# Kernel tuning notes

Hardware: AMD Instinct MI355X
Metric: run time of the kernel (lower is better)

Reference implementation:

```python
import jax, jax.numpy as jnp
import numpy as np

NUM_HEADS = 4


def setup_inputs() -> dict:
    key = jax.random.key(0)
    ks = jax.random.split(key, 5)
    B, C, L = 8, 128, 2048
    x = jax.random.normal(ks[0], (B, C, L), dtype=jnp.float32)
    # Conv1d(C, 3C, 1) == per-position linear; weight [3C, C], bias [3C]
    w_qkv = jax.random.normal(ks[1], (3 * C, C), dtype=jnp.float32) * (1.0 / np.sqrt(C))
    b_qkv = jax.random.normal(ks[2], (3 * C,), dtype=jnp.float32) * 0.01
    w_proj = jax.random.normal(ks[3], (C, C), dtype=jnp.float32) * (1.0 / np.sqrt(C))
    b_proj = jax.random.normal(ks[4], (C,), dtype=jnp.float32) * 0.01
    return {"x": x, "w_qkv": w_qkv, "b_qkv": b_qkv, "w_proj": w_proj, "b_proj": b_proj}


def reference(x, w_qkv, b_qkv, w_proj, b_proj):
    B, C, L = x.shape
    H = NUM_HEADS
    D = C // H
    scale = D ** -0.5
    # 1x1 conv qkv projection: [B, 3C, L]
    qkv = jnp.einsum('oc,bcl->bol', w_qkv, x) + b_qkv[None, :, None]
    # reshape (B,3,H,D,L) -> permute to (3,B,H,L,D)
    qkv = qkv.reshape(B, 3, H, D, L).transpose(1, 0, 2, 4, 3)
    q, k, v = qkv[0], qkv[1], qkv[2]  # each [B, H, L, D]
    attn = jax.nn.softmax(jnp.einsum('bhld,bhmd->bhlm', q, k) * scale, axis=-1)
    out = jnp.einsum('bhlm,bhmd->bhld', attn, v)  # [B, H, L, D]
    out = out.transpose(0, 1, 3, 2).reshape(B, C, L)
    out = jnp.einsum('oc,bcl->bol', w_proj, out) + b_proj[None, :, None]
    return out + x
```

## Files before the change

kernel.cpp:

```cpp
#include <hip/hip_runtime.h>

#define Bsz 8
#define Cdim 128
#define Lseq 2048
#define NH 4
#define HD 32
#define BH 32
#define QSCALE (0.17677669529663687f * 1.4426950408889634f)

typedef __bf16 bf16x8 __attribute__((ext_vector_type(8)));
typedef float f32x4 __attribute__((ext_vector_type(4)));
typedef unsigned u32x4 __attribute__((ext_vector_type(4)));

__device__ __forceinline__ float fexp2(float x) {
#if __has_builtin(__builtin_amdgcn_exp2f)
    return __builtin_amdgcn_exp2f(x);
#else
    return __expf(x * 0.6931471805599453f);
#endif
}

__device__ __forceinline__ unsigned short f2bf(float f) {
    unsigned u = __builtin_bit_cast(unsigned, f);
    u += 0x7FFFu + ((u >> 16) & 1u);
    return (unsigned short)(u >> 16);
}

__device__ __forceinline__ unsigned pack_bf16(float a, float b) {
    return (unsigned)f2bf(a) | ((unsigned)f2bf(b) << 16);
}

__device__ __forceinline__ unsigned pack_bf16_rtz(float a, float b) {
    return __builtin_amdgcn_perm(__builtin_bit_cast(unsigned, b),
                                 __builtin_bit_cast(unsigned, a), 0x07060302u);
}

__device__ __forceinline__ float bf_lo(unsigned u) {
    return __builtin_bit_cast(float, u << 16);
}
__device__ __forceinline__ float bf_hi(unsigned u) {
    return __builtin_bit_cast(float, u & 0xFFFF0000u);
}

#define MFMA16(A, B, C) __builtin_amdgcn_mfma_f32_16x16x32_bf16((A), (B), (C), 0, 0, 0)

__global__ __launch_bounds__(256) void qkv_kernel(const float* __restrict__ x,
        const float* __restrict__ w, const float* __restrict__ bias,
        unsigned short* __restrict__ qh, unsigned short* __restrict__ kh,
        unsigned short* __restrict__ vh) {
    __shared__ __attribute__((aligned(16))) unsigned short T[64][132];
    int bid = blockIdx.x;
    int og = bid % 6;
    int lt = (bid / 6) & 31;
    int b  = bid / 192;
    int l0 = lt * 64;
    int t = threadIdx.x;
    int lane = t & 63, wv = t >> 6;
    int m16 = lane & 15, quad = lane >> 4;
    int o0 = og * 64 + wv * 16;

    bf16x8 af[4];
    #pragma unroll
    for (int ks = 0; ks < 4; ks++) {
        const float* p = w + (size_t)(o0 + m16) * Cdim + ks * 32 + quad * 8;
        float4 f0 = *(const float4*)p;
        float4 f1 = *(const float4*)(p + 4);
        u32x4 u = {pack_bf16(f0.x, f0.y), pack_bf16(f0.z, f0.w),
                   pack_bf16(f1.x, f1.y), pack_bf16(f1.z, f1.w)};
        af[ks] = __builtin_bit_cast(bf16x8, u);
    }
    float bs[4];
    #pragma unroll
    for (int r = 0; r < 4; r++) bs[r] = bias[o0 + quad * 4 + r];

    {
        int ll = t & 63, cg = t >> 6;
        const float* xb = x + (size_t)b * Cdim * Lseq + l0 + ll;
        #pragma unroll
        for (int i = 0; i < 16; i++) {
            int c = cg * 32 + 2 * i;
            float f0 = xb[(size_t)c * Lseq];
            float f1 = xb[(size_t)(c + 1) * Lseq];
            *(unsigned*)&T[ll][c] = pack_bf16(f0, f1);
        }
    }
    __syncthreads();

    int oq = o0 + quad * 4;
    #pragma unroll
    for (int ns = 0; ns < 4; ns++) {
        bf16x8 bx[4];
        #pragma unroll
        for (int ks = 0; ks < 4; ks++)
            bx[ks] = *(const bf16x8*)(&T[ns * 16 + m16][ks * 32 + quad * 8]);
        f32x4 acc = {0.f, 0.f, 0.f, 0.f};
        #pragma unroll
        for (int ks = 0; ks < 4; ks++) acc = MFMA16(af[ks], bx[ks], acc);
        int l = l0 + ns * 16 + m16;
        if (og < 2) {
            int h = oq >> 5, d0 = oq & 31;
            uint2 u;
            u.x = pack_bf16((acc[0] + bs[0]) * QSCALE, (acc[1] + bs[1]) * QSCALE);
            u.y = pack_bf16((acc[2] + bs[2]) * QSCALE, (acc[3] + bs[3]) * QSCALE);
            *(uint2*)(qh + ((size_t)(b * NH + h) * Lseq + l) * HD + d0) = u;
        } else if (og < 4) {
            int o = oq - Cdim, h = o >> 5, d0 = o & 31;
            uint2 u;
            u.x = pack_bf16(acc[0] + bs[0], acc[1] + bs[1]);
            u.y = pack_bf16(acc[2] + bs[2], acc[3] + bs[3]);
            *(uint2*)(kh + ((size_t)(b * NH + h) * Lseq + l) * HD + d0) = u;
        } else {
            int kc = l >> 6, kk = l & 63;
            int half = kk >> 5, k32 = kk & 31;
            int q_, j_;
            if (k32 < 16) { q_ = k32 >> 2; j_ = k32 & 3; }
            else          { q_ = (k32 - 16) >> 2; j_ = 4 + ((k32 - 16) & 3); }
            int pos = half * 32 + q_ * 8 + j_;
            #pragma unroll
            for (int r = 0; r < 4; r++) {
                int o = oq + r - 2 * Cdim, h = o >> 5, d = o & 31;
                vh[(((size_t)(b * NH + h) * 32 + kc) * HD + d) * 64 + pos] =
                    f2bf(acc[r] + bs[r]);
            }
        }
    }
}

__global__ __launch_bounds__(256) void attn_kernel(
        const unsigned short* __restrict__ qh, const unsigned short* __restrict__ kh,
        const unsigned short* __restrict__ vh, unsigned short* __restrict__ attnb) {
    __shared__ __attribute__((aligned(16))) char smem[19456];

    int bid = blockIdx.x;
    int xcd  = bid & 7;
    int rest = bid >> 3;
    int qt = rest & 31;
    int bh = xcd + 8 * (rest >> 5);

    int lane = threadIdx.x & 63;
    int wv   = threadIdx.x >> 6;
    int m16  = lane & 15;
    int quad = lane >> 4;
    int l0 = qt * 64;

    bf16x8 qf[4];
    #pragma unroll
    for (int qs = 0; qs < 4; qs++)
        qf[qs] = *(const bf16x8*)(qh + ((size_t)bh * Lseq + l0 + qs * 16 + m16) * HD + quad * 8);

    bf16x8 ones;
    #pragma unroll
    for (int i = 0; i < 8; i++) ones[i] = (__bf16)1.0f;

    f32x4 oacc[4][2];
    f32x4 lacc[4];
    #pragma unroll
    for (int qs = 0; qs < 4; qs++) {
        oacc[qs][0] = f32x4{0.f, 0.f, 0.f, 0.f};
        oacc[qs][1] = f32x4{0.f, 0.f, 0.f, 0.f};
        lacc[qs]    = f32x4{0.f, 0.f, 0.f, 0.f};
    }
    f32x4 zero = {0.f, 0.f, 0.f, 0.f};

    const unsigned short* kb = kh + (size_t)bh * Lseq * HD + m16 * HD + quad * 8;
    const unsigned short* vb = vh + (size_t)bh * 32 * HD * 64;
    int kbase = wv * 512;

    auto load_kv = [&](int chunk, bf16x8* kf, bf16x8* vf) {
        int k0 = kbase + chunk * 64;
        #pragma unroll
        for (int t = 0; t < 4; t++)
            kf[t] = *(const bf16x8*)(kb + (size_t)(k0 + 16 * t) * HD);
        const unsigned short* vch = vb + (size_t)(k0 >> 6) * (HD * 64);
        vf[0] = *(const bf16x8*)(vch + m16 * 64 + quad * 8);
        vf[1] = *(const bf16x8*)(vch + (16 + m16) * 64 + quad * 8);
        vf[2] = *(const bf16x8*)(vch + m16 * 64 + 32 + quad * 8);
        vf[3] = *(const bf16x8*)(vch + (16 + m16) * 64 + 32 + quad * 8);
    };

    auto compute = [&](const bf16x8* kf, const bf16x8* vf) {
        #pragma unroll
        for (int qs = 0; qs < 4; qs++) {
            f32x4 s0 = MFMA16(kf[0], qf[qs], zero);
            f32x4 s1 = MFMA16(kf[1], qf[qs], zero);
            f32x4 s2 = MFMA16(kf[2], qf[qs], zero);
            f32x4 s3 = MFMA16(kf[3], qf[qs], zero);
            float p00 = fexp2(s0[0]), p01 = fexp2(s0[1]), p02 = fexp2(s0[2]), p03 = fexp2(s0[3]);
            float p10 = fexp2(s1[0]), p11 = fexp2(s1[1]), p12 = fexp2(s1[2]), p13 = fexp2(s1[3]);
            float p20 = fexp2(s2[0]), p21 = fexp2(s2[1]), p22 = fexp2(s2[2]), p23 = fexp2(s2[3]);
            float p30 = fexp2(s3[0]), p31 = fexp2(s3[1]), p32 = fexp2(s3[2]), p33 = fexp2(s3[3]);
            u32x4 lo = {pack_bf16_rtz(p00, p01), pack_bf16_rtz(p02, p03),
                        pack_bf16_rtz(p10, p11), pack_bf16_rtz(p12, p13)};
            u32x4 hi = {pack_bf16_rtz(p20, p21), pack_bf16_rtz(p22, p23),
                        pack_bf16_rtz(p30, p31), pack_bf16_rtz(p32, p33)};
            bf16x8 pfL = __builtin_bit_cast(bf16x8, lo);
            bf16x8 pfH = __builtin_bit_cast(bf16x8, hi);
            oacc[qs][0] = MFMA16(vf[0], pfL, oacc[qs][0]);
            oacc[qs][1] = MFMA16(vf[1], pfL, oacc[qs][1]);
            lacc[qs]    = MFMA16(ones,  pfL, lacc[qs]);
            oacc[qs][0] = MFMA16(vf[2], pfH, oacc[qs][0]);
            oacc[qs][1] = MFMA16(vf[3], pfH, oacc[qs][1]);
            lacc[qs]    = MFMA16(ones,  pfH, lacc[qs]);
        }
    };

    bf16x8 kA[4], vA[4], kB[4], vB[4];
    load_kv(0, kA, vA);
    load_kv(1, kB, vB);
    #pragma unroll
    for (int it = 0; it < 8; it += 2) {
        compute(kA, vA);
        load_kv(it + 2 < 8 ? it + 2 : 7, kA, vA);
        compute(kB, vB);
        load_kv(it + 3 < 8 ? it + 3 : 7, kB, vB);
    }

    unsigned* red_o = (unsigned*)smem;
    float* red_l = (float*)(smem + 18432);
    #pragma unroll
    for (int qs = 0; qs < 4; qs++) {
        int row = qs * 16 + m16;
        unsigned* rw = red_o + (size_t)(wv * 64 + row) * 18;
        *(uint2*)(rw + 2 * quad) =
            make_uint2(pack_bf16_rtz(oacc[qs][0][0], oacc[qs][0][1]),
                       pack_bf16_rtz(oacc[qs][0][2], oacc[qs][0][3]));
        *(uint2*)(rw + 8 + 2 * quad) =
            make_uint2(pack_bf16_rtz(oacc[qs][1][0], oacc[qs][1][1]),
                       pack_bf16_rtz(oacc[qs][1][2], oacc[qs][1][3]));
        if (quad == 0) red_l[wv * 64 + row] = lacc[qs][0];
    }
    __syncthreads();

    int q = threadIdx.x >> 2;
    int s4 = (threadIdx.x & 3) * 4;
    float a8[8] = {0.f, 0.f, 0.f, 0.f, 0.f, 0.f, 0.f, 0.f};
    float lt = 0.f;
    #pragma unroll
    for (int w = 0; w < 4; w++) {
        const unsigned* rr = red_o + (size_t)(w * 64 + q) * 18 + s4;
        uint2 ua = *(const uint2*)(rr);
        uint2 ub = *(const uint2*)(rr + 2);
        a8[0] += bf_lo(ua.x); a8[1] += bf_hi(ua.x);
        a8[2] += bf_lo(ua.y); a8[3] += bf_hi(ua.y);
        a8[4] += bf_lo(ub.x); a8[5] += bf_hi(ub.x);
        a8[6] += bf_lo(ub.y); a8[7] += bf_hi(ub.y);
        lt += red_l[w * 64 + q];
    }
    float inv = 1.0f / lt;
    int b = bh >> 2, h = bh & 3;
    int d0 = (threadIdx.x & 3) * 8;
    unsigned short* ob = attnb + ((size_t)b * Lseq + l0 + q) * Cdim + h * HD + d0;
    uint4 u;
    u.x = pack_bf16(a8[0] * inv, a8[1] * inv);
    u.y = pack_bf16(a8[2] * inv, a8[3] * inv);
    u.z = pack_bf16(a8[4] * inv, a8[5] * inv);
    u.w = pack_bf16(a8[6] * inv, a8[7] * inv);
    *(uint4*)ob = u;
}

__global__ __launch_bounds__(256) void proj_kernel(const float* __restrict__ wp,
        const unsigned short* __restrict__ attnb, const float* __restrict__ bias,
        const float* __restrict__ x, float* __restrict__ out) {
    int bid = blockIdx.x;
    int ot = bid & 1;
    int nt = bid >> 1;
    int lane = threadIdx.x & 63;
    int wv = threadIdx.x >> 6;
    int m16 = lane & 15, quad = lane >> 4;
    int o0 = ot * 64 + wv * 16;
    int n0 = nt * 32;

    bf16x8 af[4];
    #pragma unroll
    for (int ks = 0; ks < 4; ks++) {
        const float* p = wp + (size_t)(o0 + m16) * Cdim + ks * 32 + quad * 8;
        float4 f0 = *(const float4*)p;
        float4 f1 = *(const float4*)(p + 4);
        u32x4 u = {pack_bf16(f0.x, f0.y), pack_bf16(f0.z, f0.w),
                   pack_bf16(f1.x, f1.y), pack_bf16(f1.z, f1.w)};
        af[ks] = __builtin_bit_cast(bf16x8, u);
    }
    float bs[4];
    #pragma unroll
    for (int r = 0; r < 4; r++) bs[r] = bias[o0 + quad * 4 + r];
    int oq = o0 + quad * 4;

    #pragma unroll
    for (int lt2 = 0; lt2 < 2; lt2++) {
        int n = n0 + lt2 * 16 + m16;
        f32x4 acc = {0.f, 0.f, 0.f, 0.f};
        #pragma unroll
        for (int ks = 0; ks < 4; ks++) {
            bf16x8 bx = *(const bf16x8*)(attnb + (size_t)n * Cdim + ks * 32 + quad * 8);
            acc = MFMA16(af[ks], bx, acc);
        }
        int b = n >> 11, l = n & (Lseq - 1);
        #pragma unroll
        for (int r = 0; r < 4; r++) {
            size_t xi = ((size_t)b * Cdim + oq + r) * Lseq + l;
            out[xi] = acc[r] + bs[r] + x[xi];
        }
    }
}

extern "C" void kernel_launch(void* const* d_in, const int* in_sizes, int n_in,
                              void* d_out, int out_size, void* d_ws, size_t ws_size,
                              hipStream_t stream) {
    const float* x      = (const float*)d_in[0];
    const float* w_qkv  = (const float*)d_in[1];
    const float* b_qkv  = (const float*)d_in[2];
    const float* w_proj = (const float*)d_in[3];
    const float* b_proj = (const float*)d_in[4];
    float* out = (float*)d_out;

    const size_t E = (size_t)BH * Lseq * HD;
    unsigned short* qh    = (unsigned short*)d_ws;
    unsigned short* kh    = qh + E;
    unsigned short* vh    = kh + E;
    unsigned short* attnb = vh + E;

    qkv_kernel<<<dim3(1536), dim3(256), 0, stream>>>(x, w_qkv, b_qkv, qh, kh, vh);
    attn_kernel<<<dim3(BH * 32), dim3(256), 0, stream>>>(qh, kh, vh, attnb);
    proj_kernel<<<dim3(1024), dim3(256), 0, stream>>>(w_proj, attnb, b_proj, x, out);
}
```

Measured before the change: 121.2 us.

## Split attention key range across two blocks and merge partials in projection

The attention grid doubles to 2048 blocks, with each block covering half of the key sequence. Each block writes unnormalized fp32 partial outputs and row sums to workspace. The projection kernel then loads both halves, sums them, normalizes, converts to bf16 in shared memory and runs the MFMA projection. This raises parallelism and occupancy for attention, at the cost of extra fp32 partial traffic to and from global memory and additional work in the projection kernel.

```diff
diff --git a/kernel.cpp b/kernel.cpp
--- a/kernel.cpp
+++ b/kernel.cpp
@@ -128,14 +128,17 @@
 
 __global__ __launch_bounds__(256) void attn_kernel(
         const unsigned short* __restrict__ qh, const unsigned short* __restrict__ kh,
-        const unsigned short* __restrict__ vh, unsigned short* __restrict__ attnb) {
+        const unsigned short* __restrict__ vh, float* __restrict__ po,
+        float* __restrict__ pl) {
     __shared__ __attribute__((aligned(16))) char smem[19456];
 
     int bid = blockIdx.x;
     int xcd  = bid & 7;
     int rest = bid >> 3;
     int qt = rest & 31;
-    int bh = xcd + 8 * (rest >> 5);
+    int hb = rest >> 5;
+    int bh = xcd + 8 * (hb & 3);
+    int half = hb >> 2;
 
     int lane = threadIdx.x & 63;
     int wv   = threadIdx.x >> 6;
@@ -164,7 +167,7 @@
 
     const unsigned short* kb = kh + (size_t)bh * Lseq * HD + m16 * HD + quad * 8;
     const unsigned short* vb = vh + (size_t)bh * 32 * HD * 64;
-    int kbase = wv * 512;
+    int kbase = half * 1024 + wv * 256;
 
     auto load_kv = [&](int chunk, bf16x8* kf, bf16x8* vf) {
         int k0 = kbase + chunk * 64;
@@ -207,13 +210,12 @@
     bf16x8 kA[4], vA[4], kB[4], vB[4];
     load_kv(0, kA, vA);
     load_kv(1, kB, vB);
-    #pragma unroll
-    for (int it = 0; it < 8; it += 2) {
-        compute(kA, vA);
-        load_kv(it + 2 < 8 ? it + 2 : 7, kA, vA);
-        compute(kB, vB);
-        load_kv(it + 3 < 8 ? it + 3 : 7, kB, vB);
-    }
+    compute(kA, vA);
+    load_kv(2, kA, vA);
+    compute(kB, vB);
+    load_kv(3, kB, vB);
+    compute(kA, vA);
+    compute(kB, vB);
 
     unsigned* red_o = (unsigned*)smem;
     float* red_l = (float*)(smem + 18432);
@@ -246,29 +248,55 @@
         a8[6] += bf_lo(ub.y); a8[7] += bf_hi(ub.y);
         lt += red_l[w * 64 + q];
     }
-    float inv = 1.0f / lt;
-    int b = bh >> 2, h = bh & 3;
     int d0 = (threadIdx.x & 3) * 8;
-    unsigned short* ob = attnb + ((size_t)b * Lseq + l0 + q) * Cdim + h * HD + d0;
-    uint4 u;
-    u.x = pack_bf16(a8[0] * inv, a8[1] * inv);
-    u.y = pack_bf16(a8[2] * inv, a8[3] * inv);
-    u.z = pack_bf16(a8[4] * inv, a8[5] * inv);
-    u.w = pack_bf16(a8[6] * inv, a8[7] * inv);
-    *(uint4*)ob = u;
+    float* pob = po + ((size_t)(half * BH + bh) * Lseq + l0 + q) * HD + d0;
+    *(float4*)pob       = make_float4(a8[0], a8[1], a8[2], a8[3]);
+    *(float4*)(pob + 4) = make_float4(a8[4], a8[5], a8[6], a8[7]);
+    if ((threadIdx.x & 3) == 0)
+        pl[(size_t)(half * BH + bh) * Lseq + l0 + q] = lt;
 }
 
 __global__ __launch_bounds__(256) void proj_kernel(const float* __restrict__ wp,
-        const unsigned short* __restrict__ attnb, const float* __restrict__ bias,
-        const float* __restrict__ x, float* __restrict__ out) {
+        const float* __restrict__ po, const float* __restrict__ pl,
+        const float* __restrict__ bias, const float* __restrict__ x,
+        float* __restrict__ out) {
+    __shared__ __attribute__((aligned(16))) unsigned short T[32][132];
     int bid = blockIdx.x;
     int ot = bid & 1;
     int nt = bid >> 1;
-    int lane = threadIdx.x & 63;
-    int wv = threadIdx.x >> 6;
+    int n0 = nt * 32;
+    int t = threadIdx.x;
+
+    {
+        int nl = t >> 3, g = t & 7;
+        int h = g >> 1, d0 = (g & 1) * 16;
+        int n = n0 + nl, b = n >> 11, l = n & (Lseq - 1);
+        int bh = b * NH + h;
+        const float* p0 = po + ((size_t)bh * Lseq + l) * HD + d0;
+        const float* p1 = po + ((size_t)(BH + bh) * Lseq + l) * HD + d0;
+        float inv = 1.0f / (pl[(size_t)bh * Lseq + l] + pl[(size_t)(BH + bh) * Lseq + l]);
+        float4 a0 = *(const float4*)p0,        a1 = *(const float4*)(p0 + 4);
+        float4 a2 = *(const float4*)(p0 + 8),  a3 = *(const float4*)(p0 + 12);
+        float4 b0 = *(const float4*)p1,        b1 = *(const float4*)(p1 + 4);
+        float4 b2 = *(const float4*)(p1 + 8),  b3 = *(const float4*)(p1 + 12);
+        uint4 u0, u1;
+        u0.x = pack_bf16((a0.x + b0.x) * inv, (a0.y + b0.y) * inv);
+        u0.y = pack_bf16((a0.z + b0.z) * inv, (a0.w + b0.w) * inv);
+        u0.z = pack_bf16((a1.x + b1.x) * inv, (a1.y + b1.y) * inv);
+        u0.w = pack_bf16((a1.z + b1.z) * inv, (a1.w + b1.w) * inv);
+        u1.x = pack_bf16((a2.x + b2.x) * inv, (a2.y + b2.y) * inv);
+        u1.y = pack_bf16((a2.z + b2.z) * inv, (a2.w + b2.w) * inv);
+        u1.z = pack_bf16((a3.x + b3.x) * inv, (a3.y + b3.y) * inv);
+        u1.w = pack_bf16((a3.z + b3.z) * inv, (a3.w + b3.w) * inv);
+        int c0 = g * 16;
+        *(uint4*)&T[nl][c0]     = u0;
+        *(uint4*)&T[nl][c0 + 8] = u1;
+    }
+
+    int lane = t & 63;
+    int wv = t >> 6;
     int m16 = lane & 15, quad = lane >> 4;
     int o0 = ot * 64 + wv * 16;
-    int n0 = nt * 32;
 
     bf16x8 af[4];
     #pragma unroll
@@ -285,15 +313,18 @@
     for (int r = 0; r < 4; r++) bs[r] = bias[o0 + quad * 4 + r];
     int oq = o0 + quad * 4;
 
+    __syncthreads();
+
     #pragma unroll
     for (int lt2 = 0; lt2 < 2; lt2++) {
         int n = n0 + lt2 * 16 + m16;
+        bf16x8 bx[4];
+        #pragma unroll
+        for (int ks = 0; ks < 4; ks++)
+            bx[ks] = *(const bf16x8*)(&T[lt2 * 16 + m16][ks * 32 + quad * 8]);
         f32x4 acc = {0.f, 0.f, 0.f, 0.f};
         #pragma unroll
-        for (int ks = 0; ks < 4; ks++) {
-            bf16x8 bx = *(const bf16x8*)(attnb + (size_t)n * Cdim + ks * 32 + quad * 8);
-            acc = MFMA16(af[ks], bx, acc);
-        }
+        for (int ks = 0; ks < 4; ks++) acc = MFMA16(af[ks], bx[ks], acc);
         int b = n >> 11, l = n & (Lseq - 1);
         #pragma unroll
         for (int r = 0; r < 4; r++) {
@@ -314,12 +345,13 @@
     float* out = (float*)d_out;
 
     const size_t E = (size_t)BH * Lseq * HD;
-    unsigned short* qh    = (unsigned short*)d_ws;
-    unsigned short* kh    = qh + E;
-    unsigned short* vh    = kh + E;
-    unsigned short* attnb = vh + E;
+    unsigned short* qh = (unsigned short*)d_ws;
+    unsigned short* kh = qh + E;
+    unsigned short* vh = kh + E;
+    float* po = (float*)(vh + E);
+    float* pl = po + 2 * E;
 
     qkv_kernel<<<dim3(1536), dim3(256), 0, stream>>>(x, w_qkv, b_qkv, qh, kh, vh);
-    attn_kernel<<<dim3(BH * 32), dim3(256), 0, stream>>>(qh, kh, vh, attnb);
-    proj_kernel<<<dim3(1024), dim3(256), 0, stream>>>(w_proj, attnb, b_proj, x, out);
-}
+    attn_kernel<<<dim3(2048), dim3(256), 0, stream>>>(qh, kh, vh, po, pl);
+    proj_kernel<<<dim3(1024), dim3(256), 0, stream>>>(w_proj, po, pl, b_qkv == b_proj ? b_proj : b_proj, x, out);
+}
```

Result: no change. 123.2 us (+1.7%).
